# Optimization experiments

Hardware: AMD Instinct MI355X
Metric: run time of the kernel (lower is better)

## Reference

```python
import jax, jax.numpy as jnp
import numpy as np

N_NODES = 50000


def _laplacian_norm(edge_index, edge_weight, n):
    # PyG ChebConv normalization='sym', lambda_max=2: L_hat = L - I = -D^{-1/2} A D^{-1/2}
    # with diagonal 0 for deg>0 nodes and -1 for isolated nodes.
    row, col = edge_index[0], edge_index[1]
    deg = jax.ops.segment_sum(edge_weight, row, num_segments=n)
    dinv = jnp.where(deg > 0, jax.lax.rsqrt(jnp.where(deg > 0, deg, 1.0)), 0.0)
    norm = -edge_weight * dinv[row] * dinv[col]
    diag = jnp.where(deg > 0, 0.0, -1.0)
    return norm, diag


def _prop(x, row, col, norm, diag, n):
    # x: [N, F] -> L_hat @ x via edge gather/scatter
    return jax.ops.segment_sum(norm[:, None] * x[row], col, num_segments=n) + diag[:, None] * x


def _cheb_basis(x, K, row, col, norm, diag, n):
    # Chebyshev recursion: T0 = x, T1 = L_hat x, Tk = 2 L_hat T_{k-1} - T_{k-2}
    Tx = [x]
    if K > 1:
        Tx.append(_prop(x, row, col, norm, diag, n))
    for _ in range(2, K):
        Tx.append(2.0 * _prop(Tx[-1], row, col, norm, diag, n) - Tx[-2])
    return jnp.stack(Tx)  # [K, N, F]


def _gconv_gru_layer(X_seq, Wx, Wh, bx, bh, row, col, norm, diag, n):
    # X_seq: [T, B, N, Fin]; Wx: [3, K, Fin, H]; Wh: [3, K, H, H]; bx/bh: [3, H]
    K = Wx.shape[1]
    out_dim = Wx.shape[-1]
    B = X_seq.shape[1]
    basis = jax.vmap(lambda x: _cheb_basis(x, K, row, col, norm, diag, n))  # [B,N,F] -> [B,K,N,F]

    def step(H, X):
        TX = basis(X)  # [B,K,N,Fin]
        gx = jnp.einsum('bkni,gkio->bgno', TX, Wx) + bx[None, :, None, :]  # [B,3,N,H]
        TH = basis(H)  # [B,K,N,H]
        gz = jnp.einsum('bkno,kop->bnp', TH, Wh[0]) + bh[0]
        gr = jnp.einsum('bkno,kop->bnp', TH, Wh[1]) + bh[1]
        Z = jax.nn.sigmoid(gx[:, 0] + gz)
        R = jax.nn.sigmoid(gx[:, 1] + gr)
        THR = basis(H * R)
        gh = jnp.einsum('bkno,kop->bnp', THR, Wh[2]) + bh[2]
        H_tilde = jnp.tanh(gx[:, 2] + gh)
        Hn = Z * H + (1.0 - Z) * H_tilde
        return Hn, Hn

    H0 = jnp.zeros((B, X_seq.shape[2], out_dim), X_seq.dtype)
    _, Hs = jax.lax.scan(step, H0, X_seq)
    return Hs  # [T, B, N, H]


def setup_inputs() -> dict:
    key = jax.random.key(0)
    ks = jax.random.split(key, 16)
    B, T, N, F_in, H, K, E = 4, 12, N_NODES, 8, 32, 3, 1000000
    s = 0.05
    inp = {
        'in_tensor': jax.random.normal(ks[0], (B, T, N, F_in), jnp.float32),
        'edge_index': jax.random.randint(ks[1], (2, E), 0, N, jnp.int64),
        'edge_weight': jax.random.uniform(ks[2], (E,), jnp.float32),
        'Wx0': jax.random.normal(ks[3], (3, K, F_in, H), jnp.float32) * s,
        'Wh0': jax.random.normal(ks[4], (3, K, H, H), jnp.float32) * s,
        'bx0': jax.random.normal(ks[5], (3, H), jnp.float32) * s,
        'bh0': jax.random.normal(ks[6], (3, H), jnp.float32) * s,
        'Wx1': jax.random.normal(ks[7], (3, K, H, H), jnp.float32) * s,
        'Wh1': jax.random.normal(ks[8], (3, K, H, H), jnp.float32) * s,
        'bx1': jax.random.normal(ks[9], (3, H), jnp.float32) * s,
        'bh1': jax.random.normal(ks[10], (3, H), jnp.float32) * s,
        'mu_W': jax.random.normal(ks[11], (H, 2), jnp.float32) * s,
        'mu_b': jax.random.normal(ks[12], (2,), jnp.float32) * s,
        'sigma_W': jax.random.normal(ks[13], (H, 2), jnp.float32) * s,
        'sigma_b': jax.random.normal(ks[14], (2,), jnp.float32) * s,
    }
    return inp


def reference(in_tensor, edge_index, edge_weight, Wx0, Wh0, bx0, bh0,
              Wx1, Wh1, bx1, bh1, mu_W, mu_b, sigma_W, sigma_b):
    B, T, n = in_tensor.shape[:3]
    row, col = edge_index[0], edge_index[1]
    norm, diag = _laplacian_norm(edge_index, edge_weight, n)
    X = jnp.transpose(in_tensor, (1, 0, 2, 3))  # [T, B, N, F]
    H1 = _gconv_gru_layer(X, Wx0, Wh0, bx0, bh0, row, col, norm, diag, n)
    H2 = _gconv_gru_layer(H1, Wx1, Wh1, bx1, bh1, row, col, norm, diag, n)
    out = H2[-1]  # [B, N, hidden] -- last timestep of last layer
    mu = jax.nn.sigmoid(out @ mu_W + mu_b)
    sigma = jax.nn.softplus(out @ sigma_W + sigma_b)
    mix_coeff = jax.nn.softmax(out.mean(axis=1), axis=1)  # global mean pool over nodes
    return mu, sigma, mix_coeff
```

## Files before the change

kernel.cpp:

```cpp
#include <hip/hip_runtime.h>
#include <cstdint>
#include <cstddef>


typedef _Float16 half4 __attribute__((ext_vector_type(4)));
typedef _Float16 half8_t __attribute__((ext_vector_type(8)));
typedef float f32x4 __attribute__((ext_vector_type(4)));

__device__ __forceinline__ float sigmoidf_(float x){ return 1.f/(1.f+__expf(-x)); }


__global__ void detect_kernel(const unsigned* __restrict__ buf, int ndw, int* flag){
  int i = blockIdx.x*blockDim.x + threadIdx.x;
  int j = 2*i + 1;
  if (j < ndw && buf[j] != 0u) atomicOr(flag, 1);
}

__global__ void convert_kernel(const void* __restrict__ eidx, const float* __restrict__ w,
                               int E, const int* __restrict__ flag,
                               int* __restrict__ row32, int* __restrict__ col32,
                               float* __restrict__ deg, int* __restrict__ cnt){
  int e = blockIdx.x*blockDim.x + threadIdx.x;
  if (e >= E) return;
  int r, c;
  if (*flag){ const int* p = (const int*)eidx; r = p[e]; c = p[E+e]; }
  else { const long long* p = (const long long*)eidx; r = (int)p[e]; c = (int)p[(size_t)E+e]; }
  row32[e] = r; col32[e] = c;
  atomicAdd(deg + r, w[e]);
  atomicAdd(cnt + c, 1);
}

__global__ void node_prep_kernel(const float* __restrict__ deg, float* __restrict__ dinv,
                                 float* __restrict__ dg, int N){
  int n = blockIdx.x*blockDim.x + threadIdx.x;
  if (n >= N) return;
  float d = deg[n];
  if (d > 0.f){ dinv[n] = rsqrtf(d); dg[n] = 0.f; }
  else        { dinv[n] = 0.f;       dg[n] = -1.f; }
}

__global__ void scan_kernel(const int* __restrict__ cnt, int* __restrict__ ptrout, int N){
  __shared__ int s[1024];
  int t = threadIdx.x;
  int chunk = (N + 1023) / 1024;
  int a0 = t*chunk, a1 = min(N, a0 + chunk);
  int sum = 0;
  for (int i = a0; i < a1; ++i) sum += (cnt[i]+7)&~7;
  s[t] = sum; __syncthreads();
  for (int off = 1; off < 1024; off <<= 1){
    int v = (t >= off) ? s[t-off] : 0;
    __syncthreads();
    s[t] += v;
    __syncthreads();
  }
  int run = (t == 0) ? 0 : s[t-1];
  for (int i = a0; i < a1; ++i){ ptrout[i] = run; run += (cnt[i]+7)&~7; }
  if (t == 1023) ptrout[N] = s[1023];
}

__global__ void fill_kernel(const int* __restrict__ row32, const int* __restrict__ col32,
                            const float* __restrict__ w, const float* __restrict__ dinv,
                            const int* __restrict__ ptrv, int* __restrict__ cnt2,
                            int* __restrict__ srcs, float* __restrict__ vals, int E){
  int e = blockIdx.x*blockDim.x + threadIdx.x;
  if (e >= E) return;
  int r = row32[e], c = col32[e];
  int p = ptrv[c] + atomicAdd(cnt2 + c, 1);
  srcs[p] = r;
  vals[p] = -w[e] * dinv[r] * dinv[c];
}

__global__ void pad_kernel(const int* __restrict__ cnt, const int* __restrict__ ptrv,
                           int* __restrict__ srcs, float* __restrict__ vals, int N){
  int n = blockIdx.x*blockDim.x + threadIdx.x;
  if (n >= N) return;
  int base = ptrv[n];
  int real = cnt[n];
  int padded = ptrv[n+1] - base;
  for (int j = real; j < padded; ++j){ srcs[base+j] = 0; vals[base+j] = 0.f; }
}

__global__ __launch_bounds__(256) void spmm128h_kernel(
    const int* __restrict__ ptrv, const int* __restrict__ srcs, const float* __restrict__ vals,
    const float* __restrict__ dg, const half4* __restrict__ xh,
    half4* __restrict__ yh, int N){
  int t = threadIdx.x;
  int g = t >> 5, lane = t & 31;
  int node = blockIdx.x*8 + g;
  if (node >= N) return;
  int e0 = ptrv[node], e1 = ptrv[node+1];
  float4 acc = make_float4(0.f,0.f,0.f,0.f);
  for (int eb = e0; eb < e1; eb += 8){
    int j = eb + (lane & 7);
    int s = srcs[j]; float v = vals[j];
    #pragma unroll
    for (int q = 0; q < 8; ++q){
      int   sq = __shfl(s, q, 32);
      float vq = __shfl(v, q, 32);
      half4 hv = xh[(size_t)sq*32 + lane];
      acc.x = fmaf(vq, (float)hv.x, acc.x);
      acc.y = fmaf(vq, (float)hv.y, acc.y);
      acc.z = fmaf(vq, (float)hv.z, acc.z);
      acc.w = fmaf(vq, (float)hv.w, acc.w);
    }
  }
  size_t ii = (size_t)node*32 + lane;
  float dgn = dg[node];
  half4 xi = xh[ii];
  half4 hr;
  hr.x = (_Float16)(acc.x + dgn*(float)xi.x);
  hr.y = (_Float16)(acc.y + dgn*(float)xi.y);
  hr.z = (_Float16)(acc.z + dgn*(float)xi.z);
  hr.w = (_Float16)(acc.w + dgn*(float)xi.w);
  yh[ii] = hr;
}

__global__ __launch_bounds__(256) void spmm_dual_kernel(
    const int* __restrict__ ptrv, const int* __restrict__ srcs, const float* __restrict__ vals,
    const float* __restrict__ dg,
    const half4* __restrict__ xa, const half4* __restrict__ xb,
    const half4* __restrict__ za, const half4* __restrict__ zb,
    half4* __restrict__ ya, half4* __restrict__ yb, int N, float alpha, float beta){
  int t = threadIdx.x;
  int g = t >> 5, lane = t & 31;
  int node = blockIdx.x*8 + g;
  if (node >= N) return;
  int e0 = ptrv[node], e1 = ptrv[node+1];
  float4 aa = make_float4(0.f,0.f,0.f,0.f);
  float4 ab = make_float4(0.f,0.f,0.f,0.f);
  for (int eb = e0; eb < e1; eb += 8){
    int j = eb + (lane & 7);
    int s = srcs[j]; float v = vals[j];
    #pragma unroll
    for (int q = 0; q < 8; ++q){
      int   sq = __shfl(s, q, 32);
      float vq = __shfl(v, q, 32);
      half4 ha = xa[(size_t)sq*32 + lane];
      half4 hb = xb[(size_t)sq*32 + lane];
      aa.x = fmaf(vq, (float)ha.x, aa.x);
      aa.y = fmaf(vq, (float)ha.y, aa.y);
      aa.z = fmaf(vq, (float)ha.z, aa.z);
      aa.w = fmaf(vq, (float)ha.w, aa.w);
      ab.x = fmaf(vq, (float)hb.x, ab.x);
      ab.y = fmaf(vq, (float)hb.y, ab.y);
      ab.z = fmaf(vq, (float)hb.z, ab.z);
      ab.w = fmaf(vq, (float)hb.w, ab.w);
    }
  }
  size_t ii = (size_t)node*32 + lane;
  float dgn = dg[node];
  half4 xia = xa[ii], xib = xb[ii];
  float4 ra, rb;
  ra.x = alpha*(aa.x + dgn*(float)xia.x);
  ra.y = alpha*(aa.y + dgn*(float)xia.y);
  ra.z = alpha*(aa.z + dgn*(float)xia.z);
  ra.w = alpha*(aa.w + dgn*(float)xia.w);
  rb.x = alpha*(ab.x + dgn*(float)xib.x);
  rb.y = alpha*(ab.y + dgn*(float)xib.y);
  rb.z = alpha*(ab.z + dgn*(float)xib.z);
  rb.w = alpha*(ab.w + dgn*(float)xib.w);
  if (za){
    half4 zva = za[ii];
    half4 zvb = zb[ii];
    ra.x = fmaf(beta, (float)zva.x, ra.x); ra.y = fmaf(beta, (float)zva.y, ra.y);
    ra.z = fmaf(beta, (float)zva.z, ra.z); ra.w = fmaf(beta, (float)zva.w, ra.w);
    rb.x = fmaf(beta, (float)zvb.x, rb.x); rb.y = fmaf(beta, (float)zvb.y, rb.y);
    rb.z = fmaf(beta, (float)zvb.z, rb.z); rb.w = fmaf(beta, (float)zvb.w, rb.w);
  }
  half4 hra, hrb;
  hra.x = (_Float16)ra.x; hra.y = (_Float16)ra.y; hra.z = (_Float16)ra.z; hra.w = (_Float16)ra.w;
  hrb.x = (_Float16)rb.x; hrb.y = (_Float16)rb.y; hrb.z = (_Float16)rb.z; hrb.w = (_Float16)rb.w;
  ya[ii] = hra;
  yb[ii] = hrb;
}

__global__ __launch_bounds__(256) void spmm32h_kernel(
    const int* __restrict__ ptrv, const int* __restrict__ srcs, const float* __restrict__ vals,
    const float* __restrict__ dg, const half4* __restrict__ xh, const half4* __restrict__ z,
    half4* __restrict__ yh, int N, float alpha, float beta){
  size_t slab = (size_t)blockIdx.y * N * 8;
  const half4* xs = xh + slab;
  half4*       ys = yh + slab;
  int t = threadIdx.x;
  int g = t >> 3, lane = t & 7;
  int node = blockIdx.x*32 + g;
  if (node >= N) return;
  int e0 = ptrv[node], e1 = ptrv[node+1];
  float4 acc = make_float4(0.f,0.f,0.f,0.f);
  for (int eb = e0; eb < e1; eb += 8){
    int j = eb + lane;
    int s = srcs[j]; float v = vals[j];
    #pragma unroll
    for (int q = 0; q < 8; ++q){
      int   sq = __shfl(s, q, 8);
      float vq = __shfl(v, q, 8);
      half4 hv = xs[(size_t)sq*8 + lane];
      acc.x = fmaf(vq, (float)hv.x, acc.x);
      acc.y = fmaf(vq, (float)hv.y, acc.y);
      acc.z = fmaf(vq, (float)hv.z, acc.z);
      acc.w = fmaf(vq, (float)hv.w, acc.w);
    }
  }
  size_t ii = (size_t)node*8 + lane;
  float dgn = dg[node];
  half4 xi = xs[ii];
  float4 r;
  r.x = alpha*(acc.x + dgn*(float)xi.x);
  r.y = alpha*(acc.y + dgn*(float)xi.y);
  r.z = alpha*(acc.z + dgn*(float)xi.z);
  r.w = alpha*(acc.w + dgn*(float)xi.w);
  if (z){
    half4 zi = (z + slab)[ii];
    r.x = fmaf(beta, (float)zi.x, r.x);
    r.y = fmaf(beta, (float)zi.y, r.y);
    r.z = fmaf(beta, (float)zi.z, r.z);
    r.w = fmaf(beta, (float)zi.w, r.w);
  }
  half4 hr;
  hr.x = (_Float16)r.x; hr.y = (_Float16)r.y; hr.z = (_Float16)r.z; hr.w = (_Float16)r.w;
  ys[ii] = hr;
}

__global__ __launch_bounds__(256) void spmm_gateB_kernel(
    const int* __restrict__ ptrv, const int* __restrict__ srcs, const float* __restrict__ vals,
    const float* __restrict__ dg, const half4* __restrict__ th1h,
    const half4* __restrict__ HRbh,
    const float* __restrict__ Whh, const float* __restrict__ bhh,
    const half4* __restrict__ Zh, const half4* __restrict__ gx2h,
    half4* __restrict__ Hh, int N){
  __shared__ _Float16 sp[8][3][128];
  __shared__ float sW[3072];
  int t = threadIdx.x;
  int g = t >> 5, lane = t & 31;
  int node = blockIdx.x*8 + g;
  bool valid = (node < N);
  if (!valid) node = N-1;
  for (int idx = t; idx < 3072; idx += 256) sW[idx] = Whh[idx];
  size_t ii = (size_t)node*32 + lane;
  half4 Zvh  = Zh[ii];
  half4 Gxh  = gx2h[ii];
  half4 Holdh = Hh[ii];
  half4 zih  = HRbh[ii];
  int e0 = ptrv[node], e1 = ptrv[node+1];
  float4 acc = make_float4(0.f,0.f,0.f,0.f);
  for (int eb = e0; eb < e1; eb += 8){
    int j = eb + (lane & 7);
    int s = srcs[j]; float v = vals[j];
    #pragma unroll
    for (int q = 0; q < 8; ++q){
      int   sq = __shfl(s, q, 32);
      float vq = __shfl(v, q, 32);
      half4 hv = th1h[(size_t)sq*32 + lane];
      acc.x = fmaf(vq, (float)hv.x, acc.x);
      acc.y = fmaf(vq, (float)hv.y, acc.y);
      acc.z = fmaf(vq, (float)hv.z, acc.z);
      acc.w = fmaf(vq, (float)hv.w, acc.w);
    }
  }
  float dgn = dg[node];
  half4 xih = th1h[ii];
  half4 p2h;
  p2h.x = (_Float16)(2.f*(acc.x + dgn*(float)xih.x) - (float)zih.x);
  p2h.y = (_Float16)(2.f*(acc.y + dgn*(float)xih.y) - (float)zih.y);
  p2h.z = (_Float16)(2.f*(acc.z + dgn*(float)xih.z) - (float)zih.z);
  p2h.w = (_Float16)(2.f*(acc.w + dgn*(float)xih.w) - (float)zih.w);
  ((half4*)&sp[g][0][0])[lane] = zih;
  ((half4*)&sp[g][1][0])[lane] = xih;
  ((half4*)&sp[g][2][0])[lane] = p2h;
  __syncthreads();
  const float4* W4 = (const float4*)sW;
  float4 bv = ((const float4*)bhh)[lane & 7];
  float gh0 = bv.x, gh1 = bv.y, gh2 = bv.z, gh3 = bv.w;
  #pragma unroll 1
  for (int k = 0; k < 3; ++k){
    const _Float16* pk = &sp[g][k][(lane >> 3)*32];
    #pragma unroll
    for (int o = 0; o < 32; o += 4){
      half4 pv = *reinterpret_cast<const half4*>(pk + o);
      #pragma unroll
      for (int oo = 0; oo < 4; ++oo){
        float p = (float)pv[oo];
        float4 wv = W4[k*256 + (o+oo)*8 + (lane & 7)];
        gh0 = fmaf(p, wv.x, gh0);
        gh1 = fmaf(p, wv.y, gh1);
        gh2 = fmaf(p, wv.z, gh2);
        gh3 = fmaf(p, wv.w, gh3);
      }
    }
  }
  if (valid){
    half4 hh;
    float Ht, Z;
    Z = (float)Zvh.x; Ht = tanhf((float)Gxh.x + gh0); hh.x = (_Float16)(Z*(float)Holdh.x + (1.f - Z)*Ht);
    Z = (float)Zvh.y; Ht = tanhf((float)Gxh.y + gh1); hh.y = (_Float16)(Z*(float)Holdh.y + (1.f - Z)*Ht);
    Z = (float)Zvh.z; Ht = tanhf((float)Gxh.z + gh2); hh.z = (_Float16)(Z*(float)Holdh.z + (1.f - Z)*Ht);
    Z = (float)Zvh.w; Ht = tanhf((float)Gxh.w + gh3); hh.w = (_Float16)(Z*(float)Holdh.w + (1.f - Z)*Ht);
    Hh[ii] = hh;
  }
}

__global__ void transpose_all_kernel(const float* __restrict__ in, _Float16* __restrict__ out,
                                     int N){
  int idx = blockIdx.x*blockDim.x + threadIdx.x;
  int t = blockIdx.y;
  if (idx >= N*32) return;
  int n = idx >> 5; int r = idx & 31; int b = r >> 3; int i = r & 7;
  out[(size_t)t*N*32 + idx] = (_Float16)in[(((size_t)b*12 + t)*N + n)*8 + i];
}

__global__ void prep_weights_kernel(const float* __restrict__ Wx0, const float* __restrict__ Wx1,
                                    const float* __restrict__ Wh0, const float* __restrict__ Wh1,
                                    _Float16* __restrict__ bx8, _Float16* __restrict__ bx32,
                                    _Float16* __restrict__ bh0f, _Float16* __restrict__ bh1f){
  int t0 = threadIdx.x;
  for (int idx = t0; idx < 9216; idx += 256){
    int j = idx & 7; int l = (idx>>3)&63; int tc = idx>>9;
    int tt = tc/3, c = tc - 3*tt;
    int out = tt*16 + (l&15); int g = out>>5; int o = out&31;
    int fin = 8*(l>>4)+j;
    bx32[idx] = (_Float16)Wx1[(((g*3+c)*32+fin)<<5)+o];
  }
  for (int idx = t0; idx < 3072; idx += 256){
    int j = idx & 7; int l = (idx>>3)&63; int tt = idx>>9;
    int out = tt*16 + (l&15); int g = out>>5; int o = out&31;
    int b = l>>4;
    bx8[idx] = (b < 3) ? (_Float16)Wx0[(((g*3+b)*8+j)<<5)+o] : (_Float16)0.f;
  }
  for (int idx = t0; idx < 6144; idx += 256){
    int j = idx & 7; int l = (idx>>3)&63; int tc = idx>>9;
    int u = tc/3, c = tc - 3*u;
    int out = u*16 + (l&15); int g = out>>5; int o = out&31;
    int fin = 8*(l>>4)+j;
    bh0f[idx] = (_Float16)Wh0[(((g*3+c)*32+fin)<<5)+o];
    bh1f[idx] = (_Float16)Wh1[(((g*3+c)*32+fin)<<5)+o];
  }
}

template<int FIN>
__global__ __launch_bounds__(256) void gateA_mfma_kernel(
    const _Float16* __restrict__ x0h, const _Float16* __restrict__ x1h,
    const _Float16* __restrict__ x2h,
    const _Float16* __restrict__ h0h, const _Float16* __restrict__ h1h,
    const _Float16* __restrict__ h2h,
    const _Float16* __restrict__ BX, const float* __restrict__ bx,
    const _Float16* __restrict__ BH, const float* __restrict__ bh,
    _Float16* __restrict__ Zh, _Float16* __restrict__ gx2h,
    _Float16* __restrict__ HRbh, int M, int ntiles){
  constexpr int NXC = (FIN == 32) ? 3 : 1;
  int t = threadIdx.x;
  int lane = t & 63, wv = t >> 6;
  int l15 = lane & 15, lhi = lane >> 4;

  half8_t Bxf[6*NXC], Bhf[12];
  {
    const half8_t* p = (const half8_t*)BX;
    #pragma unroll
    for (int i = 0; i < 6*NXC; ++i) Bxf[i] = p[i*64 + lane];
    const half8_t* q = (const half8_t*)BH;
    #pragma unroll
    for (int i = 0; i < 12; ++i) Bhf[i] = q[i*64 + lane];
  }
  float bz0 = bx[l15]    + bh[l15];
  float bz1 = bx[16+l15] + bh[16+l15];
  float br0 = bx[32+l15] + bh[32+l15];
  float br1 = bx[48+l15] + bh[48+l15];
  float b20 = bx[64+l15];
  float b21 = bx[80+l15];

  int wid = blockIdx.x*4 + wv;
  int nw  = gridDim.x*4;
  for (int tile = wid; tile < ntiles; tile += nw){
    int r0 = tile << 4;
    int rowa = r0 + l15; if (rowa >= M) rowa = M - 1;

    half8_t Ax[NXC], Ah[3];
    if constexpr (FIN == 32){
      const _Float16* xm[3] = {x0h, x1h, x2h};
      #pragma unroll
      for (int c = 0; c < 3; ++c)
        Ax[c] = *reinterpret_cast<const half8_t*>(xm[c] + (size_t)rowa*32 + 8*lhi);
    } else {
      if (lhi < 3){
        const _Float16* p = (lhi == 0) ? x0h : (lhi == 1) ? x1h : x2h;
        Ax[0] = *reinterpret_cast<const half8_t*>(p + (size_t)rowa*8);
      } else {
        #pragma unroll
        for (int j = 0; j < 8; ++j) Ax[0][j] = (_Float16)0.f;
      }
    }
    {
      const _Float16* hm[3] = {h0h, h1h, h2h};
      #pragma unroll
      for (int c = 0; c < 3; ++c)
        Ah[c] = *reinterpret_cast<const half8_t*>(hm[c] + (size_t)rowa*32 + 8*lhi);
    }

    f32x4 zv = {0.f, 0.f, 0.f, 0.f};
    f32x4 CX[6], CH[4];
    #pragma unroll
    for (int i = 0; i < 6; ++i) CX[i] = zv;
    #pragma unroll
    for (int i = 0; i < 4; ++i) CH[i] = zv;

    #pragma unroll
    for (int tt = 0; tt < 6; ++tt){
      #pragma unroll
      for (int c = 0; c < NXC; ++c)
        CX[tt] = __builtin_amdgcn_mfma_f32_16x16x32_f16(Ax[c], Bxf[tt*NXC+c], CX[tt], 0, 0, 0);
    }
    #pragma unroll
    for (int u = 0; u < 4; ++u){
      #pragma unroll
      for (int c = 0; c < 3; ++c)
        CH[u] = __builtin_amdgcn_mfma_f32_16x16x32_f16(Ah[c], Bhf[u*3+c], CH[u], 0, 0, 0);
    }

    #pragma unroll
    for (int reg = 0; reg < 4; ++reg){
      int row = r0 + lhi*4 + reg;
      if (row < M){
        size_t i0 = (size_t)row*32 + l15;
        size_t i1 = i0 + 16;
        float Z0 = sigmoidf_(CX[0][reg] + CH[0][reg] + bz0);
        float Z1 = sigmoidf_(CX[1][reg] + CH[1][reg] + bz1);
        float R0 = sigmoidf_(CX[2][reg] + CH[2][reg] + br0);
        float R1 = sigmoidf_(CX[3][reg] + CH[3][reg] + br1);
        Zh[i0] = (_Float16)Z0; Zh[i1] = (_Float16)Z1;
        gx2h[i0] = (_Float16)(CX[4][reg] + b20);
        gx2h[i1] = (_Float16)(CX[5][reg] + b21);
        float hv0 = (float)h0h[i0]*R0, hv1 = (float)h0h[i1]*R1;
        HRbh[i0] = (_Float16)hv0; HRbh[i1] = (_Float16)hv1;
      }
    }
  }
}

__global__ void readout_kernel(const _Float16* __restrict__ H1, const float* __restrict__ muW,
                               const float* __restrict__ mub, const float* __restrict__ sgW,
                               const float* __restrict__ sgb, float* __restrict__ outp, int N){
  int idx = blockIdx.x*blockDim.x + threadIdx.x;
  if (idx >= 4*N) return;
  int b = idx / N, n = idx - b*N;
  const _Float16* h = H1 + (size_t)n*128 + b*32;
  float m0 = mub[0], m1 = mub[1], s0 = sgb[0], s1 = sgb[1];
  #pragma unroll
  for (int o = 0; o < 32; ++o){
    float v = (float)h[o];
    m0 = fmaf(v, muW[o*2+0], m0);
    m1 = fmaf(v, muW[o*2+1], m1);
    s0 = fmaf(v, sgW[o*2+0], s0);
    s1 = fmaf(v, sgW[o*2+1], s1);
  }
  size_t base = (size_t)(b*N + n)*2;
  outp[base]   = sigmoidf_(m0);
  outp[base+1] = sigmoidf_(m1);
  size_t sb = (size_t)8*N + base;
  outp[sb]   = (s0 > 15.f) ? s0 : log1pf(__expf(s0));
  outp[sb+1] = (s1 > 15.f) ? s1 : log1pf(__expf(s1));
}

__global__ void mean_kernel(const _Float16* __restrict__ H1, float* __restrict__ mixsum, int N){
  int t = threadIdx.x;
  int chunk = (N + gridDim.x - 1) / gridDim.x;
  int n0 = blockIdx.x*chunk, n1 = min(N, n0 + chunk);
  float acc = 0.f;
  for (int n = n0; n < n1; ++n) acc += (float)H1[(size_t)n*128 + t];
  atomicAdd(mixsum + t, acc);
}

__global__ void softmax_kernel(const float* __restrict__ mixsum, float* __restrict__ outp,
                               float invN){
  __shared__ float v[128];
  __shared__ float e[128];
  int t = threadIdx.x; int b = t >> 5;
  float m = mixsum[t]*invN;
  v[t] = m; __syncthreads();
  float mx = -1e30f;
  for (int o = 0; o < 32; ++o) mx = fmaxf(mx, v[b*32 + o]);
  float ex = __expf(m - mx);
  e[t] = ex; __syncthreads();
  float s = 0.f;
  for (int o = 0; o < 32; ++o) s += e[b*32 + o];
  outp[t] = ex / s;
}


extern "C" void kernel_launch(void* const* d_in, const int* in_sizes, int n_in,
                              void* d_out, int out_size, void* d_ws, size_t ws_size,
                              hipStream_t stream){
  const float* in0  = (const float*)d_in[0];
  const void*  eidx = d_in[1];
  const float* ew   = (const float*)d_in[2];
  const float* Wx0  = (const float*)d_in[3];
  const float* Wh0  = (const float*)d_in[4];
  const float* bx0  = (const float*)d_in[5];
  const float* bh0  = (const float*)d_in[6];
  const float* Wx1  = (const float*)d_in[7];
  const float* Wh1  = (const float*)d_in[8];
  const float* bx1  = (const float*)d_in[9];
  const float* bh1  = (const float*)d_in[10];
  const float* muW  = (const float*)d_in[11];
  const float* mub  = (const float*)d_in[12];
  const float* sgW  = (const float*)d_in[13];
  const float* sgb  = (const float*)d_in[14];
  float* outp = (float*)d_out;

  const int N = in_sizes[0] / (4*12*8);
  const int E = in_sizes[1] / 2;
  const int M = 4*N;
  const int EP = E + 8*N;

  char* w = (char*)d_ws;
  size_t off = 0;
  auto alloc = [&](size_t bytes)->void*{
    void* p = w + off;
    off += (bytes + 255) & ~(size_t)255;
    return p;
  };
  int*   csr_src = (int*)  alloc((size_t)EP*4);
  float* csr_val = (float*)alloc((size_t)EP*4);
  int*   ptrv    = (int*)  alloc((size_t)(N+1)*4);
  int*   cnt     = (int*)  alloc((size_t)N*4);
  int*   cnt2    = (int*)  alloc((size_t)N*4);
  float* deg     = (float*)alloc((size_t)N*4);
  float* dinv    = (float*)alloc((size_t)N*4);
  float* dgv     = (float*)alloc((size_t)N*4);
  int*   flag    = (int*)  alloc(256);
  float* mixsum  = (float*)alloc(512);
  half4* Zh   = (half4*)alloc((size_t)N*128*2);
  half4* gx2h = (half4*)alloc((size_t)N*128*2);
  _Float16* xa0 = (_Float16*)alloc((size_t)12*N*32*2);
  _Float16* xa1 = (_Float16*)alloc((size_t)12*N*32*2);
  _Float16* xa2 = (_Float16*)alloc((size_t)12*N*32*2);
  half4* xb1h = (half4*)alloc((size_t)N*128*2);
  half4* xb2h = (half4*)alloc((size_t)N*128*2);
  half4* th1h = (half4*)alloc((size_t)N*128*2);
  half4* th2h = (half4*)alloc((size_t)N*128*2);
  half4* HRbh = (half4*)alloc((size_t)N*128*2);
  half4* H0h  = (half4*)alloc((size_t)N*128*2);
  half4* H1h  = (half4*)alloc((size_t)N*128*2);
  _Float16* bx8w  = (_Float16*)alloc(3072*2);
  _Float16* bx32w = (_Float16*)alloc(9216*2);
  _Float16* bh0w  = (_Float16*)alloc(6144*2);
  _Float16* bh1w  = (_Float16*)alloc(6144*2);
  int* row32 = (int*)Zh;
  int* col32 = row32 + E;

  (void)hipMemsetAsync(flag,   0, 4, stream);
  (void)hipMemsetAsync(deg,    0, (size_t)N*4, stream);
  (void)hipMemsetAsync(cnt,    0, (size_t)N*4, stream);
  (void)hipMemsetAsync(cnt2,   0, (size_t)N*4, stream);
  (void)hipMemsetAsync(H0h,    0, (size_t)N*128*2, stream);
  (void)hipMemsetAsync(H1h,    0, (size_t)N*128*2, stream);
  (void)hipMemsetAsync(xb1h,   0, (size_t)N*128*2, stream);
  (void)hipMemsetAsync(xb2h,   0, (size_t)N*128*2, stream);
  (void)hipMemsetAsync(mixsum, 0, 512, stream);

  {
    int ndw = 4096;
    if (ndw > 2*E) ndw = 2*E;
    int nthread = ndw/2 + 1;
    detect_kernel<<<(nthread+255)/256, 256, 0, stream>>>((const unsigned*)eidx, ndw, flag);
  }
  convert_kernel<<<(E+255)/256, 256, 0, stream>>>(eidx, ew, E, flag, row32, col32, deg, cnt);
  node_prep_kernel<<<(N+255)/256, 256, 0, stream>>>(deg, dinv, dgv, N);
  scan_kernel<<<1, 1024, 0, stream>>>(cnt, ptrv, N);
  fill_kernel<<<(E+255)/256, 256, 0, stream>>>(row32, col32, ew, dinv, ptrv, cnt2,
                                               csr_src, csr_val, E);
  pad_kernel<<<(N+255)/256, 256, 0, stream>>>(cnt, ptrv, csr_src, csr_val, N);
  prep_weights_kernel<<<1, 256, 0, stream>>>(Wx0, Wx1, Wh0, Wh1, bx8w, bx32w, bh0w, bh1w);

  const int g128 = (N+7)/8;
  const int g32  = (N+31)/32;
  const int ntiles = (M + 15) >> 4;
  const int gMF = 512;

  {
    dim3 gT((N*32+255)/256, 12);
    transpose_all_kernel<<<gT, 256, 0, stream>>>(in0, xa0, N);
    dim3 gS(g32, 12);
    spmm32h_kernel<<<gS,256,0,stream>>>(ptrv,csr_src,csr_val,dgv,
                                        (const half4*)xa0, nullptr,
                                        (half4*)xa1, N, 1.f, 0.f);
    spmm32h_kernel<<<gS,256,0,stream>>>(ptrv,csr_src,csr_val,dgv,
                                        (const half4*)xa1, (const half4*)xa0,
                                        (half4*)xa2, N, 2.f, -1.f);
  }

  for (int t = 0; t < 12; ++t){
    const _Float16* x0t = xa0 + (size_t)t*N*32;
    const _Float16* x1t = xa1 + (size_t)t*N*32;
    const _Float16* x2t = xa2 + (size_t)t*N*32;
    gateA_mfma_kernel<8><<<gMF,256,0,stream>>>(x0t,x1t,x2t,
                                               (const _Float16*)H0h,(const _Float16*)xb1h,
                                               (const _Float16*)xb2h,
                                               bx8w,bx0, bh0w,bh0,
                                               (_Float16*)Zh,(_Float16*)gx2h,
                                               (_Float16*)HRbh, M, ntiles);
    spmm128h_kernel<<<g128,256,0,stream>>>(ptrv,csr_src,csr_val,dgv, HRbh, th1h, N);
    spmm_gateB_kernel<<<g128,256,0,stream>>>(ptrv,csr_src,csr_val,dgv, th1h, HRbh,
                                             Wh0+6144, bh0+64, Zh,gx2h, H0h, N);

    spmm_dual_kernel<<<g128,256,0,stream>>>(ptrv,csr_src,csr_val,dgv,
                                            H0h, H1h, nullptr, nullptr,
                                            xb1h, th1h, N, 1.f, 0.f);
    spmm_dual_kernel<<<g128,256,0,stream>>>(ptrv,csr_src,csr_val,dgv,
                                            xb1h, th1h, H0h, H1h,
                                            xb2h, th2h, N, 2.f, -1.f);
    gateA_mfma_kernel<32><<<gMF,256,0,stream>>>((const _Float16*)H0h,(const _Float16*)xb1h,
                                                (const _Float16*)xb2h,
                                                (const _Float16*)H1h,(const _Float16*)th1h,
                                                (const _Float16*)th2h,
                                                bx32w,bx1, bh1w,bh1,
                                                (_Float16*)Zh,(_Float16*)gx2h,
                                                (_Float16*)HRbh, M, ntiles);
    spmm128h_kernel<<<g128,256,0,stream>>>(ptrv,csr_src,csr_val,dgv, HRbh, th1h, N);
    spmm_gateB_kernel<<<g128,256,0,stream>>>(ptrv,csr_src,csr_val,dgv, th1h, HRbh,
                                             Wh1+6144, bh1+64, Zh,gx2h, H1h, N);
  }

  readout_kernel<<<(4*N+255)/256, 256, 0, stream>>>((const _Float16*)H1h,
                                                    muW, mub, sgW, sgb, outp, N);
  mean_kernel<<<256, 128, 0, stream>>>((const _Float16*)H1h, mixsum, N);
  softmax_kernel<<<1, 128, 0, stream>>>(mixsum, outp + (size_t)16*N, 1.0f/(float)N);
}
```

Measured before the change: 5.375 ms.

## Split SpMM feature columns into per-XCD slabs for L2 locality

```diff
diff --git a/kernel.cpp b/kernel.cpp
--- a/kernel.cpp
+++ b/kernel.cpp
@@ -80,39 +80,43 @@
   for (int j = real; j < padded; ++j){ srcs[base+j] = 0; vals[base+j] = 0.f; }
 }
 
-__global__ __launch_bounds__(256) void spmm128h_kernel(
+__global__ __launch_bounds__(256) void spmm128c_kernel(
     const int* __restrict__ ptrv, const int* __restrict__ srcs, const float* __restrict__ vals,
-    const float* __restrict__ dg, const half4* __restrict__ xh,
-    half4* __restrict__ yh, int N){
+    const float* __restrict__ dg, const half4* __restrict__ xc,
+    half4* __restrict__ y, int N){
+  int i = blockIdx.x;
+  int xcd = i & 7;
+  int c   = xcd >> 1;
+  int j   = (i >> 3)*2 + (xcd & 1);
   int t = threadIdx.x;
-  int g = t >> 5, lane = t & 31;
-  int node = blockIdx.x*8 + g;
+  int g = t >> 3, lane = t & 7;
+  int node = j*32 + g;
   if (node >= N) return;
+  const half4* xs = xc + (size_t)c * N * 8;
   int e0 = ptrv[node], e1 = ptrv[node+1];
   float4 acc = make_float4(0.f,0.f,0.f,0.f);
   for (int eb = e0; eb < e1; eb += 8){
-    int j = eb + (lane & 7);
-    int s = srcs[j]; float v = vals[j];
+    int jj = eb + lane;
+    int s = srcs[jj]; float v = vals[jj];
     #pragma unroll
     for (int q = 0; q < 8; ++q){
-      int   sq = __shfl(s, q, 32);
-      float vq = __shfl(v, q, 32);
-      half4 hv = xh[(size_t)sq*32 + lane];
+      int   sq = __shfl(s, q, 8);
+      float vq = __shfl(v, q, 8);
+      half4 hv = xs[(size_t)sq*8 + lane];
       acc.x = fmaf(vq, (float)hv.x, acc.x);
       acc.y = fmaf(vq, (float)hv.y, acc.y);
       acc.z = fmaf(vq, (float)hv.z, acc.z);
       acc.w = fmaf(vq, (float)hv.w, acc.w);
     }
   }
-  size_t ii = (size_t)node*32 + lane;
   float dgn = dg[node];
-  half4 xi = xh[ii];
+  half4 xi = xs[(size_t)node*8 + lane];
   half4 hr;
   hr.x = (_Float16)(acc.x + dgn*(float)xi.x);
   hr.y = (_Float16)(acc.y + dgn*(float)xi.y);
   hr.z = (_Float16)(acc.z + dgn*(float)xi.z);
   hr.w = (_Float16)(acc.w + dgn*(float)xi.w);
-  yh[ii] = hr;
+  y[(size_t)node*32 + c*8 + lane] = hr;
 }
 
 __global__ __launch_bounds__(256) void spmm_dual_kernel(
@@ -174,22 +178,28 @@
   yb[ii] = hrb;
 }
 
-__global__ __launch_bounds__(256) void spmm32h_kernel(
+__global__ __launch_bounds__(256) void spmm32x_kernel(
     const int* __restrict__ ptrv, const int* __restrict__ srcs, const float* __restrict__ vals,
     const float* __restrict__ dg, const half4* __restrict__ xh, const half4* __restrict__ z,
-    half4* __restrict__ yh, int N, float alpha, float beta){
-  size_t slab = (size_t)blockIdx.y * N * 8;
-  const half4* xs = xh + slab;
-  half4*       ys = yh + slab;
+    half4* __restrict__ yh, int N, float alpha, float beta,
+    int slab0, int two_per_xcd){
+  int i = blockIdx.x;
+  int xcd = i & 7;
+  int slab, j;
+  if (two_per_xcd){ slab = slab0 + (xcd >> 1); j = (i >> 3)*2 + (xcd & 1); }
+  else            { slab = slab0 + xcd;        j = i >> 3; }
+  size_t soff = (size_t)slab * N * 8;
+  const half4* xs = xh + soff;
+  half4*       ys = yh + soff;
   int t = threadIdx.x;
   int g = t >> 3, lane = t & 7;
-  int node = blockIdx.x*32 + g;
+  int node = j*32 + g;
   if (node >= N) return;
   int e0 = ptrv[node], e1 = ptrv[node+1];
   float4 acc = make_float4(0.f,0.f,0.f,0.f);
   for (int eb = e0; eb < e1; eb += 8){
-    int j = eb + lane;
-    int s = srcs[j]; float v = vals[j];
+    int jj = eb + lane;
+    int s = srcs[jj]; float v = vals[jj];
     #pragma unroll
     for (int q = 0; q < 8; ++q){
       int   sq = __shfl(s, q, 8);
@@ -210,7 +220,7 @@
   r.z = alpha*(acc.z + dgn*(float)xi.z);
   r.w = alpha*(acc.w + dgn*(float)xi.w);
   if (z){
-    half4 zi = (z + slab)[ii];
+    half4 zi = (z + soff)[ii];
     r.x = fmaf(beta, (float)zi.x, r.x);
     r.y = fmaf(beta, (float)zi.y, r.y);
     r.z = fmaf(beta, (float)zi.z, r.z);
@@ -224,7 +234,7 @@
 __global__ __launch_bounds__(256) void spmm_gateB_kernel(
     const int* __restrict__ ptrv, const int* __restrict__ srcs, const float* __restrict__ vals,
     const float* __restrict__ dg, const half4* __restrict__ th1h,
-    const half4* __restrict__ HRbh,
+    const half4* __restrict__ HRc,
     const float* __restrict__ Whh, const float* __restrict__ bhh,
     const half4* __restrict__ Zh, const half4* __restrict__ gx2h,
     half4* __restrict__ Hh, int N){
@@ -237,10 +247,11 @@
   if (!valid) node = N-1;
   for (int idx = t; idx < 3072; idx += 256) sW[idx] = Whh[idx];
   size_t ii = (size_t)node*32 + lane;
+  size_t iiz = (size_t)(lane >> 3)*(size_t)N*8 + (size_t)node*8 + (lane & 7);
   half4 Zvh  = Zh[ii];
   half4 Gxh  = gx2h[ii];
   half4 Holdh = Hh[ii];
-  half4 zih  = HRbh[ii];
+  half4 zih  = HRc[iiz];
   int e0 = ptrv[node], e1 = ptrv[node+1];
   float4 acc = make_float4(0.f,0.f,0.f,0.f);
   for (int eb = e0; eb < e1; eb += 8){
@@ -345,7 +356,7 @@
     const _Float16* __restrict__ BX, const float* __restrict__ bx,
     const _Float16* __restrict__ BH, const float* __restrict__ bh,
     _Float16* __restrict__ Zh, _Float16* __restrict__ gx2h,
-    _Float16* __restrict__ HRbh, int M, int ntiles){
+    _Float16* __restrict__ HRc, int M, int Nn, int ntiles){
   constexpr int NXC = (FIN == 32) ? 3 : 1;
   int t = threadIdx.x;
   int lane = t & 63, wv = t >> 6;
@@ -429,7 +440,9 @@
         gx2h[i0] = (_Float16)(CX[4][reg] + b20);
         gx2h[i1] = (_Float16)(CX[5][reg] + b21);
         float hv0 = (float)h0h[i0]*R0, hv1 = (float)h0h[i1]*R1;
-        HRbh[i0] = (_Float16)hv0; HRbh[i1] = (_Float16)hv1;
+        size_t hc = (size_t)(row & 3)*((size_t)Nn*32) + (size_t)(row >> 2)*32 + l15;
+        HRc[hc]      = (_Float16)hv0;
+        HRc[hc + 16] = (_Float16)hv1;
       }
     }
   }
@@ -535,10 +548,10 @@
   half4* xb1h = (half4*)alloc((size_t)N*128*2);
   half4* xb2h = (half4*)alloc((size_t)N*128*2);
   half4* th1h = (half4*)alloc((size_t)N*128*2);
-  half4* th2h = (half4*)alloc((size_t)N*128*2);
   half4* HRbh = (half4*)alloc((size_t)N*128*2);
   half4* H0h  = (half4*)alloc((size_t)N*128*2);
   half4* H1h  = (half4*)alloc((size_t)N*128*2);
+  half4* th2h = (half4*)alloc((size_t)N*128*2);
   _Float16* bx8w  = (_Float16*)alloc(3072*2);
   _Float16* bx32w = (_Float16*)alloc(9216*2);
   _Float16* bh0w  = (_Float16*)alloc(6144*2);
@@ -571,20 +584,28 @@
   prep_weights_kernel<<<1, 256, 0, stream>>>(Wx0, Wx1, Wh0, Wh1, bx8w, bx32w, bh0w, bh1w);
 
   const int g128 = (N+7)/8;
-  const int g32  = (N+31)/32;
+  const int nb32 = (N+31)/32;
+  const int hb   = (nb32+1)/2;
+  const int g32a = 8*nb32;
+  const int g32b = 8*hb;
   const int ntiles = (M + 15) >> 4;
   const int gMF = 512;
 
   {
     dim3 gT((N*32+255)/256, 12);
     transpose_all_kernel<<<gT, 256, 0, stream>>>(in0, xa0, N);
-    dim3 gS(g32, 12);
-    spmm32h_kernel<<<gS,256,0,stream>>>(ptrv,csr_src,csr_val,dgv,
-                                        (const half4*)xa0, nullptr,
-                                        (half4*)xa1, N, 1.f, 0.f);
-    spmm32h_kernel<<<gS,256,0,stream>>>(ptrv,csr_src,csr_val,dgv,
-                                        (const half4*)xa1, (const half4*)xa0,
-                                        (half4*)xa2, N, 2.f, -1.f);
+    spmm32x_kernel<<<g32a,256,0,stream>>>(ptrv,csr_src,csr_val,dgv,
+                                          (const half4*)xa0, nullptr,
+                                          (half4*)xa1, N, 1.f, 0.f, 0, 0);
+    spmm32x_kernel<<<g32b,256,0,stream>>>(ptrv,csr_src,csr_val,dgv,
+                                          (const half4*)xa0, nullptr,
+                                          (half4*)xa1, N, 1.f, 0.f, 8, 1);
+    spmm32x_kernel<<<g32a,256,0,stream>>>(ptrv,csr_src,csr_val,dgv,
+                                          (const half4*)xa1, (const half4*)xa0,
+                                          (half4*)xa2, N, 2.f, -1.f, 0, 0);
+    spmm32x_kernel<<<g32b,256,0,stream>>>(ptrv,csr_src,csr_val,dgv,
+                                          (const half4*)xa1, (const half4*)xa0,
+                                          (half4*)xa2, N, 2.f, -1.f, 8, 1);
   }
 
   for (int t = 0; t < 12; ++t){
@@ -596,8 +617,8 @@
                                                (const _Float16*)xb2h,
                                                bx8w,bx0, bh0w,bh0,
                                                (_Float16*)Zh,(_Float16*)gx2h,
-                                               (_Float16*)HRbh, M, ntiles);
-    spmm128h_kernel<<<g128,256,0,stream>>>(ptrv,csr_src,csr_val,dgv, HRbh, th1h, N);
+                                               (_Float16*)HRbh, M, N, ntiles);
+    spmm128c_kernel<<<g32b,256,0,stream>>>(ptrv,csr_src,csr_val,dgv, HRbh, th1h, N);
     spmm_gateB_kernel<<<g128,256,0,stream>>>(ptrv,csr_src,csr_val,dgv, th1h, HRbh,
                                              Wh0+6144, bh0+64, Zh,gx2h, H0h, N);
 
@@ -613,8 +634,8 @@
                                                 (const _Float16*)th2h,
                                                 bx32w,bx1, bh1w,bh1,
                                                 (_Float16*)Zh,(_Float16*)gx2h,
-                                                (_Float16*)HRbh, M, ntiles);
-    spmm128h_kernel<<<g128,256,0,stream>>>(ptrv,csr_src,csr_val,dgv, HRbh, th1h, N);
+                                                (_Float16*)HRbh, M, N, ntiles);
+    spmm128c_kernel<<<g32b,256,0,stream>>>(ptrv,csr_src,csr_val,dgv, HRbh, th1h, N);
     spmm_gateB_kernel<<<g128,256,0,stream>>>(ptrv,csr_src,csr_val,dgv, th1h, HRbh,
                                              Wh1+6144, bh1+64, Zh,gx2h, H1h, N);
   }
```

Result: no change. 5.405 ms (+0.6%).
